# Optimization experiments

Hardware: AMD Instinct MI355X
Metric: run time of the kernel (lower is better)

Reference implementation:

```python
import jax, jax.numpy as jnp
import numpy as np

N_NODES = 100000
N_EDGES = 1600000
IN_CH = 128
HID = 128
OUT_CH = 2
NUM_GRAPHS = 512


def _mlp_params(key, d_in, d_out):
    k1, k2 = jax.random.split(key)
    s1 = 1.0 / np.sqrt(d_in)
    s2 = 1.0 / np.sqrt(d_out)
    return (jax.random.uniform(k1, (d_in, d_out), jnp.float32, -s1, s1),
            jnp.zeros((d_out,), jnp.float32),
            jax.random.uniform(k2, (d_out, d_out), jnp.float32, -s2, s2),
            jnp.zeros((d_out,), jnp.float32))


def setup_inputs() -> dict:
    key = jax.random.key(0)
    ks = jax.random.split(key, 8)
    x = jax.random.normal(ks[0], (N_NODES, IN_CH), jnp.float32)
    edge_index = jax.random.randint(ks[1], (2, N_EDGES), 0, N_NODES, jnp.int64)
    batch = jnp.sort(jax.random.randint(ks[2], (N_NODES,), 0, NUM_GRAPHS, jnp.int64))
    w1_0, b1_0, w2_0, b2_0 = _mlp_params(ks[3], IN_CH, HID)
    w1_1, b1_1, w2_1, b2_1 = _mlp_params(ks[4], HID, HID)
    w1_2, b1_2, w2_2, b2_2 = _mlp_params(ks[5], HID, HID)
    s = 1.0 / np.sqrt(HID)
    w_lin = jax.random.uniform(ks[6], (HID, OUT_CH), jnp.float32, -s, s)
    b_lin = jnp.zeros((OUT_CH,), jnp.float32)
    return {"x": x, "edge_index": edge_index, "batch": batch,
            "w1_0": w1_0, "b1_0": b1_0, "w2_0": w2_0, "b2_0": b2_0,
            "w1_1": w1_1, "b1_1": b1_1, "w2_1": w2_1, "b2_1": b2_1,
            "w1_2": w1_2, "b1_2": b1_2, "w2_2": w2_2, "b2_2": b2_2,
            "w_lin": w_lin, "b_lin": b_lin}


def _gin_conv(x, src, dst, w1, b1, w2, b2):
    # GINConv with eps=0: MLP(x + sum_{j in N(i)} x_j)
    agg = jax.ops.segment_sum(x[src], dst, num_segments=N_NODES)  # [N, d]
    h = x + agg
    h = jax.nn.relu(h @ w1 + b1)
    return h @ w2 + b2


def reference(x, edge_index, batch,
              w1_0, b1_0, w2_0, b2_0,
              w1_1, b1_1, w2_1, b2_1,
              w1_2, b1_2, w2_2, b2_2,
              w_lin, b_lin):
    src, dst = edge_index[0], edge_index[1]
    h = _gin_conv(x, src, dst, w1_0, b1_0, w2_0, b2_0)
    h = jax.nn.relu(h)
    h = jax.nn.relu(_gin_conv(h, src, dst, w1_1, b1_1, w2_1, b2_1))
    h = jax.nn.relu(h)  # forward applies relu twice after GIN1
    h = _gin_conv(h, src, dst, w1_2, b1_2, w2_2, b2_2)
    # global mean pool per graph
    sums = jax.ops.segment_sum(h, batch, num_segments=NUM_GRAPHS)  # [G, d]
    counts = jax.ops.segment_sum(jnp.ones((N_NODES,), h.dtype), batch,
                                 num_segments=NUM_GRAPHS)
    pooled = sums / jnp.maximum(counts, 1.0)[:, None]
    # dropout is identity in eval mode
    return pooled @ w_lin + b_lin  # [G, OUT_CH]
```

## Files before the change

### kernel.cpp

```cpp
#include <hip/hip_runtime.h>
#include <hip/hip_bf16.h>

#define N_NODES   100000
#define N_EDGES   1600000
#define IN_CH     128
#define HID       128
#define OUT_CH    2
#define NUM_GRAPHS 512

#define BKT_SHIFT 9
#define NB2 ((N_NODES + 511) >> BKT_SHIFT)
#define PB  200
#define CHUNK (N_EDGES / PB)

#define NCAST (N_NODES * IN_CH / 4 / 256)

typedef __attribute__((ext_vector_type(8))) short bf16x8;
typedef __attribute__((ext_vector_type(4))) float f32x4;
typedef unsigned int uint32;
typedef unsigned long long uint64;

static __device__ __forceinline__ float b2f(uint32 b) {
    return __uint_as_float(b << 16);
}
static __device__ __forceinline__ unsigned short f2b(float f) {
    uint32 u = __float_as_uint(f);
    u += 0x7fffu + ((u >> 16) & 1u);
    return (unsigned short)(u >> 16);
}
static __device__ __forceinline__ void acc8(float* a, int4 v) {
    uint32 x;
    x = (uint32)v.x; a[0] += __uint_as_float(x << 16); a[1] += __uint_as_float(x & 0xffff0000u);
    x = (uint32)v.y; a[2] += __uint_as_float(x << 16); a[3] += __uint_as_float(x & 0xffff0000u);
    x = (uint32)v.z; a[4] += __uint_as_float(x << 16); a[5] += __uint_as_float(x & 0xffff0000u);
    x = (uint32)v.w; a[6] += __uint_as_float(x << 16); a[7] += __uint_as_float(x & 0xffff0000u);
}

__global__ void k_front(const float* __restrict__ x, unsigned short* __restrict__ h,
                        const float* w0, const float* w1, const float* w2,
                        const float* w3, const float* w4, const float* w5,
                        unsigned short* __restrict__ wt,
                        const int* __restrict__ dst, int* __restrict__ histG) {
    __shared__ int hist[NB2];
    int bid = blockIdx.x, t = threadIdx.x;
    if (bid < NCAST) {
        int base = (bid * 256 + t) * 4;
        float4 v = *(const float4*)(x + base);
        ushort4 o;
        o.x = f2b(v.x); o.y = f2b(v.y); o.z = f2b(v.z); o.w = f2b(v.w);
        *(ushort4*)(h + base) = o;
    } else if (bid < NCAST + 6) {
        const float* ws[6] = {w0, w1, w2, w3, w4, w5};
        int wi = bid - NCAST;
        const float* w = ws[wi];
        unsigned short* o = wt + wi * 16384;
        for (int i = t; i < 16384; i += 256) {
            int k = i >> 7, n = i & 127;
            o[n * 128 + k] = f2b(w[i]);
        }
    } else {
        int blk = bid - NCAST - 6;
        for (int i = t; i < NB2; i += 256) hist[i] = 0;
        __syncthreads();
        int base = blk * CHUNK;
        for (int i = t; i < CHUNK; i += 256)
            atomicAdd(&hist[dst[base + i] >> BKT_SHIFT], 1);
        __syncthreads();
        for (int i = t; i < NB2; i += 256) histG[i * PB + blk] = hist[i];
    }
}

__global__ void k_scan1(const int* __restrict__ in, int* __restrict__ out,
                        int* __restrict__ bsum, int n) {
    __shared__ int sm[256];
    int b = blockIdx.x, t = threadIdx.x;
    int base = b * 1024 + t * 4;
    int v0 = 0, v1 = 0, v2 = 0, v3 = 0;
    if (base + 3 < n) {
        int4 q = *(const int4*)(in + base);
        v0 = q.x; v1 = q.y; v2 = q.z; v3 = q.w;
    } else {
        if (base + 0 < n) v0 = in[base + 0];
        if (base + 1 < n) v1 = in[base + 1];
        if (base + 2 < n) v2 = in[base + 2];
        if (base + 3 < n) v3 = in[base + 3];
    }
    int s = v0 + v1 + v2 + v3;
    sm[t] = s;
    __syncthreads();
    for (int off = 1; off < 256; off <<= 1) {
        int u = (t >= off) ? sm[t - off] : 0;
        __syncthreads();
        sm[t] += u;
        __syncthreads();
    }
    int p = (t == 0) ? 0 : sm[t - 1];
    int o0 = p, o1 = p + v0, o2 = o1 + v1, o3 = o2 + v2;
    if (base + 3 < n) {
        *(int4*)(out + base) = make_int4(o0, o1, o2, o3);
    } else {
        if (base + 0 < n) out[base + 0] = o0;
        if (base + 1 < n) out[base + 1] = o1;
        if (base + 2 < n) out[base + 2] = o2;
        if (base + 3 < n) out[base + 3] = o3;
    }
    if (t == 255) bsum[b] = s + ((t == 0) ? 0 : sm[t - 1]);
}

__global__ void k_scan3b(int* __restrict__ out, const int* __restrict__ bsum, int n) {
    __shared__ int add_s;
    int b = blockIdx.x, t = threadIdx.x;
    if (t == 0) {
        int s = 0;
        for (int i = 0; i < b; ++i) s += bsum[i];
        add_s = s;
    }
    __syncthreads();
    int add = add_s;
    int base = b * 1024 + t * 4;
    if (base + 3 < n) {
        int4 q = *(const int4*)(out + base);
        q.x += add; q.y += add; q.z += add; q.w += add;
        *(int4*)(out + base) = q;
    } else {
        for (int j = 0; j < 4; ++j)
            if (base + j < n) out[base + j] += add;
    }
}

__global__ void k_p3g(const int* __restrict__ ei, const int* __restrict__ baseG,
                      uint64* __restrict__ ebuf,
                      const int* __restrict__ batch, int* __restrict__ goff) {
    __shared__ int cur[NB2];
    int t = threadIdx.x, blk = blockIdx.x;
    if (blk >= PB) {
        int g = (blk - PB) * 512 + t;
        if (g <= NUM_GRAPHS) {
            int lo = 0, hi = N_NODES;
            while (lo < hi) {
                int mid = (lo + hi) >> 1;
                if (batch[mid] < g) lo = mid + 1; else hi = mid;
            }
            goff[g] = lo;
        }
        return;
    }
    for (int i = t; i < NB2; i += 512) cur[i] = baseG[i * PB + blk];
    __syncthreads();
    int base = blk * CHUNK;
    for (int i = t; i < CHUNK; i += 512) {
        int e = base + i;
        int src = ei[e];
        int dst = ei[N_EDGES + e];
        int pos = atomicAdd(&cur[dst >> BKT_SHIFT], 1);
        ebuf[pos] = ((uint64)(uint32)dst << 32) | (uint32)src;
    }
}

__global__ void k_p4(const uint64* __restrict__ ebuf, const int* __restrict__ baseG,
                     int* __restrict__ off, int* __restrict__ csr) {
    __shared__ int ldeg[512];
    __shared__ int lscan[512];
    __shared__ int lcur[512];
    int b = blockIdx.x, t = threadIdx.x;
    int node0 = b << BKT_SHIFT;
    int nn = min(512, N_NODES - node0);
    int e0 = baseG[b * PB];
    int e1 = (b == NB2 - 1) ? N_EDGES : baseG[(b + 1) * PB];
    ldeg[t] = 0;
    __syncthreads();
    for (int e = e0 + t; e < e1; e += 512) {
        int dst = (int)(ebuf[e] >> 32);
        atomicAdd(&ldeg[dst - node0], 1);
    }
    __syncthreads();
    lscan[t] = ldeg[t];
    __syncthreads();
    for (int o = 1; o < 512; o <<= 1) {
        int v = (t >= o) ? lscan[t - o] : 0;
        __syncthreads();
        lscan[t] += v;
        __syncthreads();
    }
    int excl = (t == 0) ? 0 : lscan[t - 1];
    lcur[t] = e0 + excl;
    if (t < nn) off[node0 + t] = e0 + excl;
    if (b == NB2 - 1 && t == 0) off[N_NODES] = N_EDGES;
    __syncthreads();
    for (int e = e0 + t; e < e1; e += 512) {
        uint64 pr = ebuf[e];
        int dst = (int)(pr >> 32);
        int pos = atomicAdd(&lcur[dst - node0], 1);
        csr[pos] = (int)(pr & 0xffffffffu);
    }
}

template<int OUTER_RELU>
__global__ void k_gin(const unsigned short* __restrict__ h,
                      const int* __restrict__ off, const int* __restrict__ csr,
                      const unsigned short* __restrict__ w1t, const float* __restrict__ b1,
                      const unsigned short* __restrict__ w2t, const float* __restrict__ b2,
                      unsigned short* __restrict__ ho) {
    __shared__ unsigned short T[64 * 128];
    int tid = threadIdx.x;
    int lane = tid & 63, wave = tid >> 6;
    int l15 = lane & 15, l4 = lane >> 4;
    int row0 = blockIdx.x * 64;

    int g = l4, sub = l15;
    for (int r = wave * 16; r < wave * 16 + 16; ++r) {
        int node = row0 + r;
        if (node >= N_NODES) node = N_NODES - 1;
        int e0 = off[node], e1 = off[node + 1];
        float a[8] = {0.f, 0.f, 0.f, 0.f, 0.f, 0.f, 0.f, 0.f};
        int e = e0 + g;
        for (; e + 12 < e1; e += 16) {
            int s0 = csr[e], s1 = csr[e + 4], s2 = csr[e + 8], s3 = csr[e + 12];
            int4 v0 = *(const int4*)(h + (size_t)s0 * 128 + sub * 8);
            int4 v1 = *(const int4*)(h + (size_t)s1 * 128 + sub * 8);
            int4 v2 = *(const int4*)(h + (size_t)s2 * 128 + sub * 8);
            int4 v3 = *(const int4*)(h + (size_t)s3 * 128 + sub * 8);
            acc8(a, v0); acc8(a, v1); acc8(a, v2); acc8(a, v3);
        }
        for (; e + 4 < e1; e += 8) {
            int s0 = csr[e], s1 = csr[e + 4];
            int4 v0 = *(const int4*)(h + (size_t)s0 * 128 + sub * 8);
            int4 v1 = *(const int4*)(h + (size_t)s1 * 128 + sub * 8);
            acc8(a, v0); acc8(a, v1);
        }
        if (e < e1) {
            int s0 = csr[e];
            int4 v0 = *(const int4*)(h + (size_t)s0 * 128 + sub * 8);
            acc8(a, v0);
        }
#pragma unroll
        for (int j = 0; j < 8; ++j) {
            a[j] += __shfl_xor(a[j], 16);
            a[j] += __shfl_xor(a[j], 32);
        }
        if (g == 0) {
            int4 sv = *(const int4*)(h + (size_t)node * 128 + sub * 8);
            acc8(a, sv);
            int4 o;
            o.x = (int)((uint32)f2b(a[0]) | ((uint32)f2b(a[1]) << 16));
            o.y = (int)((uint32)f2b(a[2]) | ((uint32)f2b(a[3]) << 16));
            o.z = (int)((uint32)f2b(a[4]) | ((uint32)f2b(a[5]) << 16));
            o.w = (int)((uint32)f2b(a[6]) | ((uint32)f2b(a[7]) << 16));
            int byte = (r * 256 + sub * 16) ^ ((r & 7) << 4);
            *(int4*)((char*)T + byte) = o;
        }
    }
    __syncthreads();

    int wn0 = wave * 32;
    bf16x8 w1f[2][4], w2f[2][4];
#pragma unroll
    for (int nt = 0; nt < 2; ++nt)
#pragma unroll
        for (int k = 0; k < 4; ++k) {
            int o = (wn0 + nt * 16 + l15) * 128 + k * 32 + l4 * 8;
            w1f[nt][k] = *(const bf16x8*)(w1t + o);
            w2f[nt][k] = *(const bf16x8*)(w2t + o);
        }
    float bias1[2] = { b1[wn0 + l15], b1[wn0 + 16 + l15] };
    float bias2[2] = { b2[wn0 + l15], b2[wn0 + 16 + l15] };

#pragma unroll
    for (int mt = 0; mt < 4; ++mt) {
        int trow = mt * 16 + l15;
        int sw = (trow & 7) << 4;
        int rb = trow * 256 + l4 * 16;
        bf16x8 a0 = *(const bf16x8*)((const char*)T + ((rb + 0)   ^ sw));
        bf16x8 a1 = *(const bf16x8*)((const char*)T + ((rb + 64)  ^ sw));
        bf16x8 a2 = *(const bf16x8*)((const char*)T + ((rb + 128) ^ sw));
        bf16x8 a3 = *(const bf16x8*)((const char*)T + ((rb + 192) ^ sw));
        __syncthreads();
#pragma unroll
        for (int nt = 0; nt < 2; ++nt) {
            f32x4 acc = {0.f, 0.f, 0.f, 0.f};
            acc = __builtin_amdgcn_mfma_f32_16x16x32_bf16(a0, w1f[nt][0], acc, 0, 0, 0);
            acc = __builtin_amdgcn_mfma_f32_16x16x32_bf16(a1, w1f[nt][1], acc, 0, 0, 0);
            acc = __builtin_amdgcn_mfma_f32_16x16x32_bf16(a2, w1f[nt][2], acc, 0, 0, 0);
            acc = __builtin_amdgcn_mfma_f32_16x16x32_bf16(a3, w1f[nt][3], acc, 0, 0, 0);
#pragma unroll
            for (int j = 0; j < 4; ++j) {
                float v = fmaxf(acc[j] + bias1[nt], 0.f);
                int orow = mt * 16 + l4 * 4 + j;
                int ocol = wn0 + nt * 16 + l15;
                int byte = (orow * 256 + ocol * 2) ^ ((orow & 7) << 4);
                *(unsigned short*)((char*)T + byte) = f2b(v);
            }
        }
    }
    __syncthreads();

#pragma unroll
    for (int mt = 0; mt < 4; ++mt) {
        int trow = mt * 16 + l15;
        int sw = (trow & 7) << 4;
        int rb = trow * 256 + l4 * 16;
        bf16x8 t0 = *(const bf16x8*)((const char*)T + ((rb + 0)   ^ sw));
        bf16x8 t1 = *(const bf16x8*)((const char*)T + ((rb + 64)  ^ sw));
        bf16x8 t2 = *(const bf16x8*)((const char*)T + ((rb + 128) ^ sw));
        bf16x8 t3 = *(const bf16x8*)((const char*)T + ((rb + 192) ^ sw));
        __syncthreads();
#pragma unroll
        for (int nt = 0; nt < 2; ++nt) {
            f32x4 acc = {0.f, 0.f, 0.f, 0.f};
            acc = __builtin_amdgcn_mfma_f32_16x16x32_bf16(t0, w2f[nt][0], acc, 0, 0, 0);
            acc = __builtin_amdgcn_mfma_f32_16x16x32_bf16(t1, w2f[nt][1], acc, 0, 0, 0);
            acc = __builtin_amdgcn_mfma_f32_16x16x32_bf16(t2, w2f[nt][2], acc, 0, 0, 0);
            acc = __builtin_amdgcn_mfma_f32_16x16x32_bf16(t3, w2f[nt][3], acc, 0, 0, 0);
#pragma unroll
            for (int j = 0; j < 4; ++j) {
                float v = acc[j] + bias2[nt];
                if (OUTER_RELU) v = fmaxf(v, 0.f);
                int orow = mt * 16 + l4 * 4 + j;
                int ocol = wn0 + nt * 16 + l15;
                int byte = (orow * 256 + ocol * 2) ^ ((orow & 7) << 4);
                *(unsigned short*)((char*)T + byte) = f2b(v);
            }
        }
    }
    __syncthreads();

    for (int c = tid; c < 1024; c += 256) {
        int r = c >> 4, cc = c & 15;
        int byte = (r * 256 + cc * 16) ^ ((r & 7) << 4);
        int4 v = *(const int4*)((const char*)T + byte);
        int gr = row0 + r;
        if (gr < N_NODES)
            *(int4*)(ho + (size_t)gr * 128 + cc * 8) = v;
    }
}

__global__ void k_pool(const unsigned short* __restrict__ h,
                       const int* __restrict__ goff,
                       const float* __restrict__ wl, const float* __restrict__ bl,
                       float* __restrict__ out) {
    __shared__ float sm[4][64][2];
    int g = blockIdx.x;
    int tid = threadIdx.x;
    int wave = tid >> 6, lane = tid & 63;
    int e0 = goff[g], e1 = goff[g + 1];
    int c2 = lane << 1;
    float s0 = 0.f, s1 = 0.f;
    int r = e0 + wave;
    for (; r + 4 < e1; r += 8) {
        uint32 v0 = *(const uint32*)(h + (size_t)r * 128 + c2);
        uint32 v1 = *(const uint32*)(h + (size_t)(r + 4) * 128 + c2);
        s0 += b2f(v0 & 0xffffu) + b2f(v1 & 0xffffu);
        s1 += b2f(v0 >> 16) + b2f(v1 >> 16);
    }
    if (r < e1) {
        uint32 v = *(const uint32*)(h + (size_t)r * 128 + c2);
        s0 += b2f(v & 0xffffu);
        s1 += b2f(v >> 16);
    }
    sm[wave][lane][0] = s0;
    sm[wave][lane][1] = s1;
    __syncthreads();
    if (wave == 0) {
        s0 = sm[0][lane][0] + sm[1][lane][0] + sm[2][lane][0] + sm[3][lane][0];
        s1 = sm[0][lane][1] + sm[1][lane][1] + sm[2][lane][1] + sm[3][lane][1];
        float inv = 1.f / fmaxf((float)(e1 - e0), 1.f);
        s0 *= inv; s1 *= inv;
        float o0 = s0 * wl[c2 * 2]     + s1 * wl[(c2 + 1) * 2];
        float o1 = s0 * wl[c2 * 2 + 1] + s1 * wl[(c2 + 1) * 2 + 1];
#pragma unroll
        for (int d = 32; d; d >>= 1) {
            o0 += __shfl_down(o0, d);
            o1 += __shfl_down(o1, d);
        }
        if (lane == 0) {
            out[g * 2]     = o0 + bl[0];
            out[g * 2 + 1] = o1 + bl[1];
        }
    }
}

extern "C" void kernel_launch(void* const* d_in, const int* in_sizes, int n_in,
                              void* d_out, int out_size, void* d_ws, size_t ws_size,
                              hipStream_t stream) {
    const float* x     = (const float*)d_in[0];
    const int*   ei    = (const int*)d_in[1];
    const int*   batch = (const int*)d_in[2];
    const float* w1[3] = {(const float*)d_in[3],  (const float*)d_in[7],  (const float*)d_in[11]};
    const float* b1[3] = {(const float*)d_in[4],  (const float*)d_in[8],  (const float*)d_in[12]};
    const float* w2[3] = {(const float*)d_in[5],  (const float*)d_in[9],  (const float*)d_in[13]};
    const float* b2[3] = {(const float*)d_in[6],  (const float*)d_in[10], (const float*)d_in[14]};
    const float* wl    = (const float*)d_in[15];
    const float* bl    = (const float*)d_in[16];

    char* p = (char*)d_ws;
    auto alloc = [&](size_t bytes) {
        char* r = p;
        p += (bytes + 255) & ~(size_t)255;
        return r;
    };
    int* off    = (int*)alloc((size_t)(N_NODES + 1) * 4);
    int* goff   = (int*)alloc((size_t)(NUM_GRAPHS + 1) * 4);
    int* histG  = (int*)alloc((size_t)(NB2 * PB) * 4);
    int* baseG  = (int*)alloc((size_t)(NB2 * PB + 1) * 4);
    int* bsum   = (int*)alloc((size_t)128 * 4);
    int* csr    = (int*)alloc((size_t)N_EDGES * 4);
    unsigned short* wts = (unsigned short*)alloc((size_t)6 * 16384 * 2);
    unsigned short* hA  = (unsigned short*)alloc((size_t)N_NODES * 128 * 2);
    unsigned short* hS  = (unsigned short*)alloc((size_t)N_NODES * 128 * 2);
    unsigned short* hB  = (unsigned short*)alloc((size_t)N_NODES * 128 * 2);
    uint64* ebuf = (uint64*)hS;

    k_front<<<NCAST + 6 + PB, 256, 0, stream>>>(x, hA,
        w1[0], w2[0], w1[1], w2[1], w1[2], w2[2], wts, ei + N_EDGES, histG);

    const int SCAN_N = NB2 * PB;
    const int SCAN_BLOCKS = (SCAN_N + 1023) / 1024;
    k_scan1<<<SCAN_BLOCKS, 256, 0, stream>>>(histG, baseG, bsum, SCAN_N);
    k_scan3b<<<SCAN_BLOCKS, 256, 0, stream>>>(baseG, bsum, SCAN_N);
    k_p3g<<<PB + 2, 512, 0, stream>>>(ei, baseG, ebuf, batch, goff);
    k_p4<<<NB2, 512, 0, stream>>>(ebuf, baseG, off, csr);

    unsigned short* wt1[3] = {wts,             wts + 2 * 16384, wts + 4 * 16384};
    unsigned short* wt2[3] = {wts + 1 * 16384, wts + 3 * 16384, wts + 5 * 16384};

    const int GIN_GRID = (N_NODES + 63) / 64;

    k_gin<1><<<GIN_GRID, 256, 0, stream>>>(hA, off, csr, wt1[0], b1[0], wt2[0], b2[0], hB);
    k_gin<1><<<GIN_GRID, 256, 0, stream>>>(hB, off, csr, wt1[1], b1[1], wt2[1], b2[1], hA);
    k_gin<0><<<GIN_GRID, 256, 0, stream>>>(hA, off, csr, wt1[2], b1[2], wt2[2], b2[2], hB);

    k_pool<<<NUM_GRAPHS, 256, 0, stream>>>(hB, goff, wl, bl, (float*)d_out);
}
```

Measured before the change: 394.5 us.

## Split fused GIN layer into separate aggregation and MLP kernels

Each fused GIN kernel is replaced by two kernels. The first is a gather-sum kernel with one wave per node, which writes the aggregated bf16 rows to a scratch buffer. The second is an MFMA MLP kernel that loads 64 rows from that buffer into swizzled LDS. The goal is more parallelism and better latency hiding for the irregular gather, which the fused kernel ran serially at 16 rows per wave. The cost is an extra global write and read of the 100000x128 intermediate per layer, plus extra kernel launches.

New measurement: 327.9 us. 1.2x faster.

```diff
diff --git a/kernel.cpp b/kernel.cpp
--- a/kernel.cpp
+++ b/kernel.cpp
@@ -195,9 +195,56 @@
     }
 }
 
+__global__ void k_agg(const unsigned short* __restrict__ h,
+                      const int* __restrict__ off, const int* __restrict__ csr,
+                      unsigned short* __restrict__ hs) {
+    int wid = (blockIdx.x * 256 + threadIdx.x) >> 6;
+    int lane = threadIdx.x & 63;
+    if (wid >= N_NODES) return;
+    int g = lane >> 4, sub = lane & 15;
+    int e0 = off[wid], e1 = off[wid + 1];
+    float a[8] = {0.f, 0.f, 0.f, 0.f, 0.f, 0.f, 0.f, 0.f};
+    int e = e0 + g;
+    for (; e + 12 < e1; e += 16) {
+        int s0 = csr[e], s1 = csr[e + 4], s2 = csr[e + 8], s3 = csr[e + 12];
+        int4 v0 = *(const int4*)(h + (size_t)s0 * 128 + sub * 8);
+        int4 v1 = *(const int4*)(h + (size_t)s1 * 128 + sub * 8);
+        int4 v2 = *(const int4*)(h + (size_t)s2 * 128 + sub * 8);
+        int4 v3 = *(const int4*)(h + (size_t)s3 * 128 + sub * 8);
+        acc8(a, v0); acc8(a, v1); acc8(a, v2); acc8(a, v3);
+    }
+    for (; e + 4 < e1; e += 8) {
+        int s0 = csr[e];
+        int s1 = csr[e + 4];
+        int4 v0 = *(const int4*)(h + (size_t)s0 * 128 + sub * 8);
+        int4 v1 = *(const int4*)(h + (size_t)s1 * 128 + sub * 8);
+        acc8(a, v0);
+        acc8(a, v1);
+    }
+    if (e < e1) {
+        int s0 = csr[e];
+        int4 v0 = *(const int4*)(h + (size_t)s0 * 128 + sub * 8);
+        acc8(a, v0);
+    }
+#pragma unroll
+    for (int j = 0; j < 8; ++j) {
+        a[j] += __shfl_xor(a[j], 16);
+        a[j] += __shfl_xor(a[j], 32);
+    }
+    if (g == 0) {
+        int4 sv = *(const int4*)(h + (size_t)wid * 128 + sub * 8);
+        acc8(a, sv);
+        int4 o;
+        o.x = (int)((uint32)f2b(a[0]) | ((uint32)f2b(a[1]) << 16));
+        o.y = (int)((uint32)f2b(a[2]) | ((uint32)f2b(a[3]) << 16));
+        o.z = (int)((uint32)f2b(a[4]) | ((uint32)f2b(a[5]) << 16));
+        o.w = (int)((uint32)f2b(a[6]) | ((uint32)f2b(a[7]) << 16));
+        *(int4*)(hs + (size_t)wid * 128 + sub * 8) = o;
+    }
+}
+
 template<int OUTER_RELU>
-__global__ void k_gin(const unsigned short* __restrict__ h,
-                      const int* __restrict__ off, const int* __restrict__ csr,
+__global__ void k_mlp(const unsigned short* __restrict__ hs,
                       const unsigned short* __restrict__ w1t, const float* __restrict__ b1,
                       const unsigned short* __restrict__ w2t, const float* __restrict__ b2,
                       unsigned short* __restrict__ ho) {
@@ -206,53 +253,17 @@
     int lane = tid & 63, wave = tid >> 6;
     int l15 = lane & 15, l4 = lane >> 4;
     int row0 = blockIdx.x * 64;
-
-    int g = l4, sub = l15;
-    for (int r = wave * 16; r < wave * 16 + 16; ++r) {
-        int node = row0 + r;
-        if (node >= N_NODES) node = N_NODES - 1;
-        int e0 = off[node], e1 = off[node + 1];
-        float a[8] = {0.f, 0.f, 0.f, 0.f, 0.f, 0.f, 0.f, 0.f};
-        int e = e0 + g;
-        for (; e + 12 < e1; e += 16) {
-            int s0 = csr[e], s1 = csr[e + 4], s2 = csr[e + 8], s3 = csr[e + 12];
-            int4 v0 = *(const int4*)(h + (size_t)s0 * 128 + sub * 8);
-            int4 v1 = *(const int4*)(h + (size_t)s1 * 128 + sub * 8);
-            int4 v2 = *(const int4*)(h + (size_t)s2 * 128 + sub * 8);
-            int4 v3 = *(const int4*)(h + (size_t)s3 * 128 + sub * 8);
-            acc8(a, v0); acc8(a, v1); acc8(a, v2); acc8(a, v3);
-        }
-        for (; e + 4 < e1; e += 8) {
-            int s0 = csr[e], s1 = csr[e + 4];
-            int4 v0 = *(const int4*)(h + (size_t)s0 * 128 + sub * 8);
-            int4 v1 = *(const int4*)(h + (size_t)s1 * 128 + sub * 8);
-            acc8(a, v0); acc8(a, v1);
-        }
-        if (e < e1) {
-            int s0 = csr[e];
-            int4 v0 = *(const int4*)(h + (size_t)s0 * 128 + sub * 8);
-            acc8(a, v0);
-        }
-#pragma unroll
-        for (int j = 0; j < 8; ++j) {
-            a[j] += __shfl_xor(a[j], 16);
-            a[j] += __shfl_xor(a[j], 32);
-        }
-        if (g == 0) {
-            int4 sv = *(const int4*)(h + (size_t)node * 128 + sub * 8);
-            acc8(a, sv);
-            int4 o;
-            o.x = (int)((uint32)f2b(a[0]) | ((uint32)f2b(a[1]) << 16));
-            o.y = (int)((uint32)f2b(a[2]) | ((uint32)f2b(a[3]) << 16));
-            o.z = (int)((uint32)f2b(a[4]) | ((uint32)f2b(a[5]) << 16));
-            o.w = (int)((uint32)f2b(a[6]) | ((uint32)f2b(a[7]) << 16));
-            int byte = (r * 256 + sub * 16) ^ ((r & 7) << 4);
-            *(int4*)((char*)T + byte) = o;
-        }
-    }
-    __syncthreads();
-
     int wn0 = wave * 32;
+
+    for (int c = tid; c < 1024; c += 256) {
+        int r = c >> 4, cc = c & 15;
+        int gr = row0 + r;
+        if (gr >= N_NODES) gr = N_NODES - 1;
+        int4 v = *(const int4*)(hs + (size_t)gr * 128 + cc * 8);
+        int byte = (r * 256 + cc * 16) ^ ((r & 7) << 4);
+        *(int4*)((char*)T + byte) = v;
+    }
+
     bf16x8 w1f[2][4], w2f[2][4];
 #pragma unroll
     for (int nt = 0; nt < 2; ++nt)
@@ -264,6 +275,7 @@
         }
     float bias1[2] = { b1[wn0 + l15], b1[wn0 + 16 + l15] };
     float bias2[2] = { b2[wn0 + l15], b2[wn0 + 16 + l15] };
+    __syncthreads();
 
 #pragma unroll
     for (int mt = 0; mt < 4; ++mt) {
@@ -423,11 +435,15 @@
     unsigned short* wt1[3] = {wts,             wts + 2 * 16384, wts + 4 * 16384};
     unsigned short* wt2[3] = {wts + 1 * 16384, wts + 3 * 16384, wts + 5 * 16384};
 
-    const int GIN_GRID = (N_NODES + 63) / 64;
-
-    k_gin<1><<<GIN_GRID, 256, 0, stream>>>(hA, off, csr, wt1[0], b1[0], wt2[0], b2[0], hB);
-    k_gin<1><<<GIN_GRID, 256, 0, stream>>>(hB, off, csr, wt1[1], b1[1], wt2[1], b2[1], hA);
-    k_gin<0><<<GIN_GRID, 256, 0, stream>>>(hA, off, csr, wt1[2], b1[2], wt2[2], b2[2], hB);
+    const int AGG_GRID = N_NODES / 4;
+    const int MLP_GRID = (N_NODES + 63) / 64;
+
+    k_agg<<<AGG_GRID, 256, 0, stream>>>(hA, off, csr, hS);
+    k_mlp<1><<<MLP_GRID, 256, 0, stream>>>(hS, wt1[0], b1[0], wt2[0], b2[0], hB);
+    k_agg<<<AGG_GRID, 256, 0, stream>>>(hB, off, csr, hS);
+    k_mlp<1><<<MLP_GRID, 256, 0, stream>>>(hS, wt1[1], b1[1], wt2[1], b2[1], hA);
+    k_agg<<<AGG_GRID, 256, 0, stream>>>(hA, off, csr, hS);
+    k_mlp<0><<<MLP_GRID, 256, 0, stream>>>(hS, wt1[2], b1[2], wt2[2], b2[2], hB);
 
     k_pool<<<NUM_GRAPHS, 256, 0, stream>>>(hB, goff, wl, bl, (float*)d_out);
 }
```
